# Kernel tuning notes

Measured on AMD Instinct MI355X. Metric: run time of the kernel, lower is better.

Reference implementation:

```python
import jax, jax.numpy as jnp
import numpy as np

HIDDEN, NQ, NKV, HD, INTER = 2048, 8, 1, 256, 8192
B, S = 4, 2048
EPS = 1e-6
ROPE_BASE = 10000.0


def ada_rms(x, t, w, tw):
    # x: (b,s,h), t: (b,h). RMS-normalize, then modulate gain with time embedding:
    # out = normed * w * (1 + t @ tw.T)
    n = x * jax.lax.rsqrt(jnp.mean(jnp.square(x), axis=-1, keepdims=True) + EPS)
    scale = t @ tw.T  # (b,h)
    return n * (w * (1.0 + scale))[:, None, :]


def apply_rope(x, pos_ids):
    # x: (b,nh,s,hd), pos_ids: (b,s)
    half = HD // 2
    inv_freq = 1.0 / (ROPE_BASE ** (jnp.arange(0, HD, 2, dtype=jnp.float32) / HD))  # (hd/2,)
    ang = pos_ids.astype(jnp.float32)[:, :, None] * inv_freq  # (b,s,hd/2)
    cos = jnp.concatenate([jnp.cos(ang), jnp.cos(ang)], axis=-1)[:, None]  # (b,1,s,hd)
    sin = jnp.concatenate([jnp.sin(ang), jnp.sin(ang)], axis=-1)[:, None]
    x1, x2 = x[..., :half], x[..., half:]
    rot = jnp.concatenate([-x2, x1], axis=-1)
    return x * cos + rot * sin


def setup_inputs() -> dict:
    key = jax.random.key(0)
    ks = jax.random.split(key, 12)
    f32 = jnp.float32
    inp = {
        "x": jax.random.normal(ks[0], (B, S, HIDDEN), f32),
        "pos_ids": jnp.broadcast_to(jnp.arange(S, dtype=jnp.int32), (B, S)),
        "time_emb": jax.random.normal(ks[1], (B, HIDDEN), f32),
        "ln1_w": jnp.ones((HIDDEN,), f32),
        "ln1_tw": jax.random.normal(ks[2], (HIDDEN, HIDDEN), f32) * 0.02,
        "ln2_w": jnp.ones((HIDDEN,), f32),
        "ln2_tw": jax.random.normal(ks[3], (HIDDEN, HIDDEN), f32) * 0.02,
        "Wq": jax.random.normal(ks[4], (NQ * HD, HIDDEN), f32) * 0.02,
        "Wk": jax.random.normal(ks[5], (NKV * HD, HIDDEN), f32) * 0.02,
        "Wv": jax.random.normal(ks[6], (NKV * HD, HIDDEN), f32) * 0.02,
        "Wo": jax.random.normal(ks[7], (HIDDEN, NQ * HD), f32) * 0.02,
        "Wg": jax.random.normal(ks[8], (INTER, HIDDEN), f32) * 0.02,
        "Wu": jax.random.normal(ks[9], (INTER, HIDDEN), f32) * 0.02,
        "Wd": jax.random.normal(ks[10], (HIDDEN, INTER), f32) * 0.02,
    }
    return inp


def reference(x, pos_ids, time_emb, ln1_w, ln1_tw, ln2_w, ln2_tw,
              Wq, Wk, Wv, Wo, Wg, Wu, Wd):
    b, s, _ = x.shape
    g = NQ // NKV  # kv groups
    res = x
    h = ada_rms(x, time_emb, ln1_w, ln1_tw)
    q = (h @ Wq.T).reshape(b, s, NQ, HD).transpose(0, 2, 1, 3)   # (b,nq,s,hd)
    k = (h @ Wk.T).reshape(b, s, NKV, HD).transpose(0, 2, 1, 3)  # (b,nkv,s,hd)
    v = (h @ Wv.T).reshape(b, s, NKV, HD).transpose(0, 2, 1, 3)
    q = apply_rope(q, pos_ids)
    k = apply_rope(k, pos_ids)
    # GQA: group query heads over shared kv heads without materializing expanded k/v
    qg = q.reshape(b, NKV, g, s, HD)
    scores = jnp.einsum("bkgsd,bktd->bkgst", qg, k) / jnp.sqrt(jnp.float32(HD))
    attn = jax.nn.softmax(scores, axis=-1)  # (b,nkv,g,s,s) — full, no causal mask
    ctx = jnp.einsum("bkgst,bktd->bkgsd", attn, v)
    ctx = ctx.reshape(b, NQ, s, HD).transpose(0, 2, 1, 3).reshape(b, s, NQ * HD)
    x = res + ctx @ Wo.T
    res = x
    h = ada_rms(x, time_emb, ln2_w, ln2_tw)
    mlp = (jax.nn.silu(h @ Wg.T) * (h @ Wu.T)) @ Wd.T
    return res + mlp
```

## Files before the change

### kernel.cpp

```cpp
#include <hip/hip_runtime.h>

typedef unsigned short u16;
typedef unsigned int   u32;
typedef __bf16  bf16x8 __attribute__((ext_vector_type(8)));
typedef float   f32x4  __attribute__((ext_vector_type(4)));
typedef u16     u16x4  __attribute__((ext_vector_type(4)));
typedef u16     u16x8  __attribute__((ext_vector_type(8)));

#define HID 2048
#define SEQ 2048
#define BB  4
#define NQH 8
#define HD_ 256
#define INTER_ 8192

__device__ __forceinline__ float b2f(u16 u) {
  union { float f; u32 i; } x; x.i = ((u32)u) << 16; return x.f;
}
__device__ __forceinline__ u16 f2b(float f) {
  u32 u = __float_as_uint(f);
  u32 r = u + 0x7fffu + ((u >> 16) & 1u);
  return (u16)(r >> 16);
}
__device__ __forceinline__ float wsum(float v) {
#pragma unroll
  for (int m = 1; m < 64; m <<= 1) v += __shfl_xor(v, m, 64);
  return v;
}
__device__ __forceinline__ float wmax(float v) {
#pragma unroll
  for (int m = 1; m < 64; m <<= 1) v = fmaxf(v, __shfl_xor(v, m, 64));
  return v;
}
__device__ __forceinline__ void gload_lds16(const void* gp, void* lp) {
  __builtin_amdgcn_global_load_lds(
      (const __attribute__((address_space(1))) void*)gp,
      (__attribute__((address_space(3))) void*)lp, 16, 0, 0);
}
__device__ __forceinline__ void xcd_swizzle(int& bx, int& by) {
  const int nx = gridDim.x, ny = gridDim.y;
  const int nwg = nx * ny;
  if ((nwg & 7) == 0) {
    const int orig = by * nx + bx;
    const int q = nwg >> 3;
    const int wg = (orig & 7) * q + (orig >> 3);
    bx = wg % nx; by = wg / nx;
  }
}

__global__ __launch_bounds__(256) void cvt_kernel(const float* __restrict__ src,
                                                  u16* __restrict__ dst, int n4) {
  int i = blockIdx.x * 256 + threadIdx.x;
  if (i < n4) {
    const float4 v = *(const float4*)(src + (size_t)i * 4);
    u16x4 o;
    o[0] = f2b(v.x); o[1] = f2b(v.y); o[2] = f2b(v.z); o[3] = f2b(v.w);
    *(u16x4*)(dst + (size_t)i * 4) = o;
  }
}

__global__ __launch_bounds__(256) void scale_kernel(
    const float* __restrict__ temb,
    const float* __restrict__ w1, const float* __restrict__ tw1,
    const float* __restrict__ w2, const float* __restrict__ tw2,
    float* __restrict__ sf1, float* __restrict__ sf2) {
  const int wave = threadIdx.x >> 6, lane = threadIdx.x & 63;
  const int o = blockIdx.x * 4 + wave;
  const int set = o / (BB * HID);
  const int r = o % (BB * HID);
  const int b = r / HID, n = r % HID;
  const float* tw = set ? tw2 : tw1;
  const float* w  = set ? w2  : w1;
  float* sf       = set ? sf2 : sf1;
  const float* tv  = temb + (size_t)b * HID;
  const float* twr = tw + (size_t)n * HID;
  float acc = 0.f;
#pragma unroll
  for (int q = 0; q < 8; ++q) {
    const float4 a = *(const float4*)(tv + q * 256 + lane * 4);
    const float4 c = *(const float4*)(twr + q * 256 + lane * 4);
    acc += a.x * c.x + a.y * c.y + a.z * c.z + a.w * c.w;
  }
  acc = wsum(acc);
  if (lane == 0) sf[(size_t)b * HID + n] = w[n] * (1.0f + acc);
}

__global__ __launch_bounds__(256) void rope_table_kernel(const int* __restrict__ pos_ids,
                                                         float* __restrict__ cosT,
                                                         float* __restrict__ sinT) {
  const int idx = blockIdx.x * 256 + threadIdx.x;
  const int j = idx & 127, bs = idx >> 7;
  const float pos = (float)pos_ids[bs];
  const float inv = exp2f(-(float)j * (13.287712379549449f / 128.0f));
  const float ang = pos * inv;
  float sv, cv;
  sincosf(ang, &sv, &cv);
  cosT[idx] = cv; sinT[idx] = sv;
}

__global__ __launch_bounds__(256) void rmsnorm_kernel(const float* __restrict__ xin,
                                                      const float* __restrict__ sfac,
                                                      u16* __restrict__ out) {
  const int row = blockIdx.x;
  const int b = row >> 11;
  const float* xr = xin + (size_t)row * HID + threadIdx.x * 8;
  const float4 v0 = *(const float4*)(xr);
  const float4 v1 = *(const float4*)(xr + 4);
  float v[8] = {v0.x, v0.y, v0.z, v0.w, v1.x, v1.y, v1.z, v1.w};
  float ss = 0.f;
#pragma unroll
  for (int j = 0; j < 8; ++j) ss += v[j] * v[j];
  ss = wsum(ss);
  __shared__ float red[4];
  const int wave = threadIdx.x >> 6, lane = threadIdx.x & 63;
  if (lane == 0) red[wave] = ss;
  __syncthreads();
  const float tot = red[0] + red[1] + red[2] + red[3];
  const float rs = rsqrtf(tot * (1.0f / HID) + 1e-6f);
  const float* sf = sfac + (size_t)b * HID + threadIdx.x * 8;
  u16* op = out + (size_t)row * HID + threadIdx.x * 8;
  u16x8 o;
#pragma unroll
  for (int j = 0; j < 8; ++j) o[j] = f2b(v[j] * rs * sf[j]);
  *(u16x8*)op = o;
}

template <int EPI>
__global__ __launch_bounds__(256) void gemm_bt(const u16* __restrict__ A,
                                               const u16* __restrict__ B,
                                               const float* __restrict__ Res,
                                               void* __restrict__ Cv,
                                               int K, int lda, int ldb, int ldc,
                                               size_t aZ, size_t cZ) {
  A += blockIdx.z * aZ;
  __shared__ u16 As[3][128 * 32];
  __shared__ u16 Bs[3][128 * 32];
  int bx = blockIdx.x, by = blockIdx.y;
  xcd_swizzle(bx, by);
  const int m0 = bx * 128, n0 = by * 128;
  const int wave = threadIdx.x >> 6, lane = threadIdx.x & 63;
  const int wr = wave >> 1, wc = wave & 1;
  const int l15 = lane & 15, l4 = lane >> 4;

  const int c0 = threadIdx.x,        r0 = c0 >> 2, u0 = c0 & 3;
  const int c1 = threadIdx.x + 256,  r1 = c1 >> 2, u1 = c1 & 3;
  const int s0 = (u0 ^ ((r0 >> 1) & 3)) << 3;
  const int s1 = (u1 ^ ((r1 >> 1) & 3)) << 3;

  auto stage = [&](int buf, int kt) {
    gload_lds16(A + (size_t)(m0 + r0) * lda + kt + s0, &As[buf][c0 * 8]);
    gload_lds16(B + (size_t)(n0 + r0) * ldb + kt + s0, &Bs[buf][c0 * 8]);
    gload_lds16(A + (size_t)(m0 + r1) * lda + kt + s1, &As[buf][c1 * 8]);
    gload_lds16(B + (size_t)(n0 + r1) * ldb + kt + s1, &Bs[buf][c1 * 8]);
  };

  f32x4 acc[4][4] = {};

  stage(0, 0);
  stage(1, 32);
  int cur = 0;
  for (int kt = 0; kt < K; kt += 32) {
    if (kt + 32 < K) {
      asm volatile("s_waitcnt vmcnt(4)" ::: "memory");
    } else {
      asm volatile("s_waitcnt vmcnt(0)" ::: "memory");
    }
    __builtin_amdgcn_s_barrier();
    if (kt + 64 < K) {
      const int nxt = (cur == 0) ? 2 : cur - 1;
      stage(nxt, kt + 64);
    }
    bf16x8 af[4], bf[4];
#pragma unroll
    for (int ms = 0; ms < 4; ++ms) {
      const int r = wr * 64 + ms * 16 + l15;
      af[ms] = *(const bf16x8*)(&As[cur][r * 32 + ((l4 ^ ((r >> 1) & 3)) << 3)]);
    }
#pragma unroll
    for (int ns = 0; ns < 4; ++ns) {
      const int r = wc * 64 + ns * 16 + l15;
      bf[ns] = *(const bf16x8*)(&Bs[cur][r * 32 + ((l4 ^ ((r >> 1) & 3)) << 3)]);
    }
#pragma unroll
    for (int ms = 0; ms < 4; ++ms)
#pragma unroll
      for (int ns = 0; ns < 4; ++ns)
        acc[ms][ns] = __builtin_amdgcn_mfma_f32_16x16x32_bf16(af[ms], bf[ns], acc[ms][ns], 0, 0, 0);
    cur = (cur == 2) ? 0 : cur + 1;
  }

  u16* Cb = (u16*)Cv + blockIdx.z * cZ;
  float* Cf = (float*)Cv + blockIdx.z * cZ;
#pragma unroll
  for (int ms = 0; ms < 4; ++ms)
#pragma unroll
    for (int i = 0; i < 4; ++i) {
      const int row = m0 + wr * 64 + ms * 16 + l4 * 4 + i;
#pragma unroll
      for (int ns = 0; ns < 4; ++ns) {
        const int col = n0 + wc * 64 + ns * 16 + l15;
        const size_t idx = (size_t)row * ldc + col;
        const float v = acc[ms][ns][i];
        if constexpr (EPI == 0) {
          Cb[idx] = f2b(v);
        } else if constexpr (EPI == 1) {
          const float g = b2f(Cb[idx]);
          Cb[idx] = f2b(g / (1.0f + __expf(-g)) * v);
        } else if constexpr (EPI == 2) {
          Cf[idx] = v + Res[idx];
        } else {
          Cf[idx] = v + Cf[idx];
        }
      }
    }
}

__global__ __launch_bounds__(256) void rope_apply_kernel(u16* __restrict__ qkv,
                                                         const float* __restrict__ cosT,
                                                         const float* __restrict__ sinT,
                                                         u16* __restrict__ vt) {
  const int tok = blockIdx.x;
  const int b = tok >> 11, s = tok & 2047;
  u16* rowp = qkv + (size_t)tok * 2560;
  const float* ct = cosT + (size_t)tok * 128;
  const float* st = sinT + (size_t)tok * 128;
  for (int p = threadIdx.x; p < 1024; p += 256) {
    const int h = p >> 7, j = p & 127;
    u16* e = rowp + h * 256 + j;
    const float x1 = b2f(e[0]), x2 = b2f(e[128]);
    const float c = ct[j], sn = st[j];
    e[0]   = f2b((x1 * c - x2 * sn) * 0.0625f);
    e[128] = f2b((x2 * c + x1 * sn) * 0.0625f);
  }
  if (threadIdx.x < 128) {
    const int j = threadIdx.x;
    u16* e = rowp + 2048 + j;
    const float x1 = b2f(e[0]), x2 = b2f(e[128]);
    const float c = ct[j], sn = st[j];
    e[0]   = f2b(x1 * c - x2 * sn);
    e[128] = f2b(x2 * c + x1 * sn);
  }
  {
    const int d = threadIdx.x;
    vt[((size_t)b * HD_ + d) * SEQ + s] = rowp[2304 + d];
  }
}

__global__ __launch_bounds__(256) void softmax_kernel(u16* __restrict__ Sb) {
  const int row = blockIdx.x;
  u16* rp = Sb + (size_t)row * 2048 + threadIdx.x * 8;
  const u16x8 t = *(const u16x8*)rp;
  float v[8];
#pragma unroll
  for (int j = 0; j < 8; ++j) v[j] = b2f(t[j]);
  float m = v[0];
#pragma unroll
  for (int j = 1; j < 8; ++j) m = fmaxf(m, v[j]);
  m = wmax(m);
  __shared__ float redm[4], reds[4];
  const int wave = threadIdx.x >> 6, lane = threadIdx.x & 63;
  if (lane == 0) redm[wave] = m;
  __syncthreads();
  m = fmaxf(fmaxf(redm[0], redm[1]), fmaxf(redm[2], redm[3]));
  float s = 0.f;
#pragma unroll
  for (int j = 0; j < 8; ++j) { v[j] = __expf(v[j] - m); s += v[j]; }
  s = wsum(s);
  if (lane == 0) reds[wave] = s;
  __syncthreads();
  const float inv = 1.0f / (reds[0] + reds[1] + reds[2] + reds[3]);
  u16x8 o;
#pragma unroll
  for (int j = 0; j < 8; ++j) o[j] = f2b(v[j] * inv);
  *(u16x8*)rp = o;
}

extern "C" void kernel_launch(void* const* d_in, const int* in_sizes, int n_in,
                              void* d_out, int out_size, void* d_ws, size_t ws_size,
                              hipStream_t stream) {
  const float* x     = (const float*)d_in[0];
  const int*   pos   = (const int*)d_in[1];
  const float* temb  = (const float*)d_in[2];
  const float* ln1w  = (const float*)d_in[3];
  const float* ln1tw = (const float*)d_in[4];
  const float* ln2w  = (const float*)d_in[5];
  const float* ln2tw = (const float*)d_in[6];
  const float* Wq    = (const float*)d_in[7];
  const float* Wk    = (const float*)d_in[8];
  const float* Wv    = (const float*)d_in[9];
  const float* Wo    = (const float*)d_in[10];
  const float* Wg    = (const float*)d_in[11];
  const float* Wu    = (const float*)d_in[12];
  const float* Wd    = (const float*)d_in[13];
  float* out = (float*)d_out;

  char* ws = (char*)d_ws;
  constexpr size_t OFF_SF1  = 0;
  constexpr size_t OFF_SF2  = 32768;
  constexpr size_t OFF_COS  = 65536;
  constexpr size_t OFF_SIN  = 4259840;
  constexpr size_t OFF_WQKV = 8454144;
  constexpr size_t OFF_WO   = 18939904;
  constexpr size_t OFF_WG   = 27328512;
  constexpr size_t OFF_WU   = 60882944;
  constexpr size_t OFF_WD   = 94437376;
  constexpr size_t OFF_H    = 127991808;
  constexpr size_t OFF_QKV  = 161546240;
  constexpr size_t OFF_VT   = 203489280;
  constexpr size_t OFF_CTX  = 207683584;
  constexpr size_t REQUIRED = 241238016;

  float* sf1 = (float*)(ws + OFF_SF1);
  float* sf2 = (float*)(ws + OFF_SF2);
  float* cosT = (float*)(ws + OFF_COS);
  float* sinT = (float*)(ws + OFF_SIN);
  u16* wqkv = (u16*)(ws + OFF_WQKV);
  u16* wo   = (u16*)(ws + OFF_WO);
  u16* wg   = (u16*)(ws + OFF_WG);
  u16* wu   = (u16*)(ws + OFF_WU);
  u16* wd   = (u16*)(ws + OFF_WD);
  u16* hbuf = (u16*)(ws + OFF_H);
  u16* qkv  = (u16*)(ws + OFF_QKV);
  u16* vt   = (u16*)(ws + OFF_VT);
  u16* ctx  = (u16*)(ws + OFF_CTX);
  u16* inter = (u16*)(ws + OFF_QKV);
  u16* Sbuf = (u16*)d_out;

  if (ws_size < REQUIRED) return;

  auto cvt = [&](const float* s, u16* d, size_t n) {
    int n4 = (int)(n / 4);
    cvt_kernel<<<(n4 + 255) / 256, 256, 0, stream>>>(s, d, n4);
  };

  cvt(Wq, wqkv,                      (size_t)2048 * HID);
  cvt(Wk, wqkv + (size_t)2048 * HID, (size_t)256 * HID);
  cvt(Wv, wqkv + (size_t)2304 * HID, (size_t)256 * HID);
  cvt(Wo, wo, (size_t)HID * HID);
  cvt(Wg, wg, (size_t)INTER_ * HID);
  cvt(Wu, wu, (size_t)INTER_ * HID);
  cvt(Wd, wd, (size_t)HID * INTER_);

  scale_kernel<<<(2 * BB * HID) / 4, 256, 0, stream>>>(temb, ln1w, ln1tw, ln2w, ln2tw, sf1, sf2);
  rope_table_kernel<<<(BB * SEQ * 128) / 256, 256, 0, stream>>>(pos, cosT, sinT);

  rmsnorm_kernel<<<BB * SEQ, 256, 0, stream>>>(x, sf1, hbuf);

  gemm_bt<0><<<dim3(64, 20), 256, 0, stream>>>(hbuf, wqkv, nullptr, qkv, HID, HID, HID, 2560, 0, 0);

  rope_apply_kernel<<<BB * SEQ, 256, 0, stream>>>(qkv, cosT, sinT, vt);

  for (int b = 0; b < BB; ++b) {
    const u16* qb = qkv + (size_t)b * SEQ * 2560;
    const u16* kb = qb + 2048;
    const u16* vb = vt + (size_t)b * HD_ * SEQ;
    u16* cb = ctx + (size_t)b * SEQ * HID;
    gemm_bt<0><<<dim3(16, 16, 8), 256, 0, stream>>>(
        qb, kb, nullptr, Sbuf, HD_, 2560, 2560, SEQ, (size_t)HD_, (size_t)SEQ * SEQ);
    softmax_kernel<<<NQH * SEQ, 256, 0, stream>>>(Sbuf);
    gemm_bt<0><<<dim3(16, 2, 8), 256, 0, stream>>>(
        Sbuf, vb, nullptr, cb, SEQ, SEQ, SEQ, HID, (size_t)SEQ * SEQ, (size_t)HD_);
  }

  gemm_bt<2><<<dim3(64, 16), 256, 0, stream>>>(ctx, wo, x, out, HID, HID, HID, HID, 0, 0);

  rmsnorm_kernel<<<BB * SEQ, 256, 0, stream>>>(out, sf2, hbuf);

  constexpr int MC = BB * SEQ / 2;
  for (int c = 0; c < 2; ++c) {
    const u16* hA = hbuf + (size_t)c * MC * HID;
    float* outC = out + (size_t)c * MC * HID;
    gemm_bt<0><<<dim3(MC / 128, INTER_ / 128), 256, 0, stream>>>(hA, wg, nullptr, inter, HID, HID, HID, INTER_, 0, 0);
    gemm_bt<1><<<dim3(MC / 128, INTER_ / 128), 256, 0, stream>>>(hA, wu, nullptr, inter, HID, HID, HID, INTER_, 0, 0);
    gemm_bt<3><<<dim3(MC / 128, HID / 128),    256, 0, stream>>>(inter, wd, nullptr, outC, INTER_, INTER_, INTER_, HID, 0, 0);
  }

  (void)in_sizes; (void)n_in; (void)out_size;
}
```

Before: 1.976 ms.

## Add 256x256-tile 512-thread GEMM kernel for QKV, Wo, gate and up projections

```diff
diff --git a/kernel.cpp b/kernel.cpp
--- a/kernel.cpp
+++ b/kernel.cpp
@@ -123,6 +123,98 @@
 #pragma unroll
   for (int j = 0; j < 8; ++j) o[j] = f2b(v[j] * rs * sf[j]);
   *(u16x8*)op = o;
+}
+
+template <int EPI>
+__global__ __launch_bounds__(512, 2) void gemm256(const u16* __restrict__ A,
+                                                  const u16* __restrict__ B,
+                                                  const float* __restrict__ Res,
+                                                  void* __restrict__ Cv,
+                                                  int K, int lda, int ldb, int ldc) {
+  __shared__ u16 As[2 * 2 * 8192];
+  __shared__ u16 Bs[2 * 2 * 8192];
+  int bx = blockIdx.x, by = blockIdx.y;
+  xcd_swizzle(bx, by);
+  const int m0 = bx * 256, n0 = by * 256;
+  const int w = threadIdx.x >> 6, lane = threadIdx.x & 63;
+  const int wr = w >> 2, wcn = w & 3;
+  const int l15 = lane & 15, l4 = lane >> 4;
+
+  const int u0 = threadIdx.x, u1 = threadIdx.x + 512;
+  const int r0 = u0 >> 2, q0 = u0 & 3, s0 = (q0 ^ ((r0 >> 1) & 3)) * 8;
+  const int r1 = u1 >> 2, q1 = u1 & 3, s1 = (q1 ^ ((r1 >> 1) & 3)) * 8;
+
+  auto stageA = [&](int buf, int ks, int kt) {
+    u16* lp = &As[(buf * 2 + ks) * 8192];
+    gload_lds16(A + (size_t)(m0 + r0) * lda + kt + ks * 32 + s0, lp + u0 * 8);
+    gload_lds16(A + (size_t)(m0 + r1) * lda + kt + ks * 32 + s1, lp + u1 * 8);
+  };
+  auto stageB = [&](int buf, int ks, int kt) {
+    u16* lp = &Bs[(buf * 2 + ks) * 8192];
+    gload_lds16(B + (size_t)(n0 + r0) * ldb + kt + ks * 32 + s0, lp + u0 * 8);
+    gload_lds16(B + (size_t)(n0 + r1) * ldb + kt + ks * 32 + s1, lp + u1 * 8);
+  };
+
+  f32x4 acc[8][4] = {};
+
+  stageA(0, 0, 0); stageB(0, 0, 0); stageA(0, 1, 0); stageB(0, 1, 0);
+
+  const int T = K >> 6;
+  for (int t = 0; t < T; ++t) {
+    const int cur = t & 1, kt = t * 64;
+    const bool more = (t + 1 < T);
+#pragma unroll
+    for (int ks = 0; ks < 2; ++ks) {
+      if (more || ks == 0) asm volatile("s_waitcnt vmcnt(4)" ::: "memory");
+      else                 asm volatile("s_waitcnt vmcnt(0)" ::: "memory");
+      __builtin_amdgcn_s_barrier();
+      asm volatile("" ::: "memory");
+      const u16* la = &As[(cur * 2 + ks) * 8192];
+      const u16* lb = &Bs[(cur * 2 + ks) * 8192];
+      bf16x8 af[8], bf[4];
+#pragma unroll
+      for (int mr = 0; mr < 8; ++mr) {
+        const int r = wr * 128 + mr * 16 + l15;
+        af[mr] = *(const bf16x8*)(la + r * 32 + ((l4 ^ ((r >> 1) & 3)) * 8));
+      }
+#pragma unroll
+      for (int nr = 0; nr < 4; ++nr) {
+        const int r = wcn * 64 + nr * 16 + l15;
+        bf[nr] = *(const bf16x8*)(lb + r * 32 + ((l4 ^ ((r >> 1) & 3)) * 8));
+      }
+      if (more) { stageA(cur ^ 1, ks, kt + 64); stageB(cur ^ 1, ks, kt + 64); }
+      __builtin_amdgcn_s_setprio(1);
+#pragma unroll
+      for (int mr = 0; mr < 8; ++mr)
+#pragma unroll
+        for (int nr = 0; nr < 4; ++nr)
+          acc[mr][nr] = __builtin_amdgcn_mfma_f32_16x16x32_bf16(af[mr], bf[nr], acc[mr][nr], 0, 0, 0);
+      __builtin_amdgcn_s_setprio(0);
+    }
+  }
+
+  u16* Cb = (u16*)Cv;
+  float* Cf = (float*)Cv;
+#pragma unroll
+  for (int mr = 0; mr < 8; ++mr)
+#pragma unroll
+    for (int i = 0; i < 4; ++i) {
+      const int row = m0 + wr * 128 + mr * 16 + l4 * 4 + i;
+#pragma unroll
+      for (int nr = 0; nr < 4; ++nr) {
+        const int col = n0 + wcn * 64 + nr * 16 + l15;
+        const size_t idx = (size_t)row * ldc + col;
+        const float v = acc[mr][nr][i];
+        if constexpr (EPI == 0) {
+          Cb[idx] = f2b(v);
+        } else if constexpr (EPI == 1) {
+          const float g = b2f(Cb[idx]);
+          Cb[idx] = f2b(g / (1.0f + __expf(-g)) * v);
+        } else {
+          Cf[idx] = v + Res[idx];
+        }
+      }
+    }
 }
 
 template <int EPI>
@@ -346,7 +438,7 @@
 
   rmsnorm_kernel<<<BB * SEQ, 256, 0, stream>>>(x, sf1, hbuf);
 
-  gemm_bt<0><<<dim3(64, 20), 256, 0, stream>>>(hbuf, wqkv, nullptr, qkv, HID, HID, HID, 2560, 0, 0);
+  gemm256<0><<<dim3(32, 10), 512, 0, stream>>>(hbuf, wqkv, nullptr, qkv, HID, HID, HID, 2560);
 
   rope_apply_kernel<<<BB * SEQ, 256, 0, stream>>>(qkv, cosT, sinT, vt);
 
@@ -362,7 +454,7 @@
         Sbuf, vb, nullptr, cb, SEQ, SEQ, SEQ, HID, (size_t)SEQ * SEQ, (size_t)HD_);
   }
 
-  gemm_bt<2><<<dim3(64, 16), 256, 0, stream>>>(ctx, wo, x, out, HID, HID, HID, HID, 0, 0);
+  gemm256<2><<<dim3(32, 8), 512, 0, stream>>>(ctx, wo, x, out, HID, HID, HID, HID);
 
   rmsnorm_kernel<<<BB * SEQ, 256, 0, stream>>>(out, sf2, hbuf);
 
@@ -370,9 +462,9 @@
   for (int c = 0; c < 2; ++c) {
     const u16* hA = hbuf + (size_t)c * MC * HID;
     float* outC = out + (size_t)c * MC * HID;
-    gemm_bt<0><<<dim3(MC / 128, INTER_ / 128), 256, 0, stream>>>(hA, wg, nullptr, inter, HID, HID, HID, INTER_, 0, 0);
-    gemm_bt<1><<<dim3(MC / 128, INTER_ / 128), 256, 0, stream>>>(hA, wu, nullptr, inter, HID, HID, HID, INTER_, 0, 0);
-    gemm_bt<3><<<dim3(MC / 128, HID / 128),    256, 0, stream>>>(inter, wd, nullptr, outC, INTER_, INTER_, INTER_, HID, 0, 0);
+    gemm256<0><<<dim3(MC / 256, INTER_ / 256), 512, 0, stream>>>(hA, wg, nullptr, inter, HID, HID, HID, INTER_);
+    gemm256<1><<<dim3(MC / 256, INTER_ / 256), 512, 0, stream>>>(hA, wu, nullptr, inter, HID, HID, HID, INTER_);
+    gemm_bt<3><<<dim3(MC / 128, HID / 128), 256, 0, stream>>>(inter, wd, nullptr, outC, INTER_, INTER_, INTER_, HID, 0, 0);
   }
 
   (void)in_sizes; (void)n_in; (void)out_size;
```

New measurement: 1.732 ms. -12.3%, faster.
